# Optimization experiments

Measured on AMD Instinct MI355X. Metric: run time of the kernel, lower is better.

## Reference

```python
import jax, jax.numpy as jnp
import numpy as np

B, S, D = 2, 2048, 2048
H, HD = 16, 128  # n_heads, head_dim = dim // n_heads
NEG_INF = -1e9


def setup_inputs() -> dict:
    key = jax.random.key(0)
    ks = jax.random.split(key, 6)
    x = jax.random.normal(ks[0], (B, S, D), dtype=jnp.float32)
    # freqs_complex as (real, imag) pairs; unused downstream because the
    # source's apply_rotary_emb returns its input unchanged (x.type_as(x)).
    freqs_complex = jax.random.normal(ks[1], (S, HD // 2, 2), dtype=jnp.float32)
    # causal additive mask [1, 1, S, S]
    causal = jnp.tril(jnp.ones((S, S), dtype=bool))
    mask = jnp.where(causal, 0.0, NEG_INF).astype(jnp.float32)[None, None]
    wq = jax.random.normal(ks[2], (D, D), dtype=jnp.float32) * 0.02
    wk = jax.random.normal(ks[3], (D, D), dtype=jnp.float32) * 0.02
    wv = jax.random.normal(ks[4], (D, D), dtype=jnp.float32) * 0.02
    wo = jax.random.normal(ks[5], (D, D), dtype=jnp.float32) * 0.02
    return {"x": x, "freqs_complex": freqs_complex, "mask": mask,
            "wq": wq, "wk": wk, "wv": wv, "wo": wo}


def reference(x, freqs_complex, mask, wq, wk, wv, wo):
    b, s, d = x.shape
    # QKV projections (torch Linear: x @ W.T), reshape to [B, S, H, HD]
    q = (x @ wq.T).reshape(b, s, H, HD)
    k = (x @ wk.T).reshape(b, s, H, HD)
    v = (x @ wv.T).reshape(b, s, H, HD)
    # apply_rotary_emb in the source returns its input unchanged -> no-op.
    scale = 1.0 / jnp.sqrt(jnp.asarray(HD, dtype=x.dtype))
    scores = jnp.einsum('bshd,bthd->bhst', q, k) * scale + mask
    probs = jax.nn.softmax(scores.astype(jnp.float32), axis=-1).astype(q.dtype)
    out = jnp.einsum('bhst,bthd->bshd', probs, v).reshape(b, s, H * HD)
    return out @ wo.T
```

## Files before the change

### kernel.cpp

```cpp
#include <hip/hip_runtime.h>
#include <hip/hip_bf16.h>
#include <stdint.h>


namespace {

constexpr int kB = 2;
constexpr int kS = 2048;
constexpr int kD = 2048;
constexpr int kH = 16;
constexpr int kHD = 128;
constexpr int kM = kB * kS;

typedef __attribute__((ext_vector_type(8))) __bf16 bf16x8;
typedef __attribute__((ext_vector_type(4))) float f32x4;

__device__ __forceinline__ unsigned short f2bf(float x) {
  uint32_t u = __float_as_uint(x);
  u += 0x7fffu + ((u >> 16) & 1u);
  return (unsigned short)(u >> 16);
}

__device__ __forceinline__ void gld_lds16(const void* g, void* l) {
  __builtin_amdgcn_global_load_lds((__attribute__((address_space(1))) void*)g,
                                   (__attribute__((address_space(3))) void*)l,
                                   16, 0, 0);
}

__global__ void cvt_all(const float* __restrict__ x, const float* __restrict__ wq,
                        const float* __restrict__ wk, const float* __restrict__ wv,
                        const float* __restrict__ wo, unsigned short* __restrict__ xb,
                        unsigned short* __restrict__ wqkv) {
  constexpr int n4 = kD * kD / 4;
  const int i = blockIdx.x * blockDim.x + threadIdx.x;
  const int y = blockIdx.y;
  const float* src;
  unsigned short* dst;
  float s = 1.0f;
  if (y < 2) {
    src = x + (size_t)y * n4 * 4;
    dst = xb + (size_t)y * n4 * 4;
  } else {
    src = (y == 2) ? wq : (y == 3) ? wk : (y == 4) ? wv : wo;
    dst = wqkv + (size_t)(y - 2) * n4 * 4;
    if (y == 2) s = 0.08838834764831845f * 1.44269504088896340736f;
  }
  float4 v = ((const float4*)src)[i];
  ushort4 o;
  o.x = f2bf(v.x * s); o.y = f2bf(v.y * s); o.z = f2bf(v.z * s); o.w = f2bf(v.w * s);
  ((ushort4*)dst)[i] = o;
}

__global__ __launch_bounds__(256, 2) void gemm_qkv(
    const unsigned short* __restrict__ A, const unsigned short* __restrict__ W,
    unsigned short* __restrict__ Qb, unsigned short* __restrict__ Kb,
    unsigned short* __restrict__ Vt) {
  constexpr int K = 2048;
  __shared__ unsigned short Asm[128 * 64];
  __shared__ unsigned short Bsm[128 * 64];
  const int t = threadIdx.x;
  const int wave = t >> 6, lane = t & 63;
  const int ln = lane & 15, quad = lane >> 4;
  const int wr = wave >> 1, wc = wave & 1;
  const int m0 = blockIdx.y * 128, n0 = blockIdx.x * 128;

  const int srow = t >> 3;
  const int scol = ((t & 7) ^ (srow & 7)) << 3;
  const unsigned short* gA = A + (size_t)(m0 + srow) * K + scol;
  const unsigned short* gW = W + (size_t)(n0 + srow) * K + scol;
  const size_t g32 = (size_t)32 * K;
  unsigned short* lA = Asm + wave * 512;
  unsigned short* lB = Bsm + wave * 512;

  f32x4 acc[4][4] = {};

  for (int k0 = 0; k0 < K; k0 += 64) {
    __syncthreads();
#pragma unroll
    for (int i = 0; i < 4; ++i) {
      gld_lds16(gA + i * g32, lA + i * 2048);
      gld_lds16(gW + i * g32, lB + i * 2048);
    }
    gA += 64; gW += 64;
    __syncthreads();

#pragma unroll
    for (int kk = 0; kk < 2; ++kk) {
      bf16x8 af[4], bw[4];
#pragma unroll
      for (int mt = 0; mt < 4; ++mt) {
        const int row = wr * 64 + mt * 16 + ln;
        af[mt] = *(const bf16x8*)(Asm + row * 64 +
                                  (((kk * 4 + quad) ^ (row & 7)) << 3));
      }
#pragma unroll
      for (int nt = 0; nt < 4; ++nt) {
        const int row = wc * 64 + nt * 16 + ln;
        bw[nt] = *(const bf16x8*)(Bsm + row * 64 +
                                  (((kk * 4 + quad) ^ (row & 7)) << 3));
      }
#pragma unroll
      for (int mt = 0; mt < 4; ++mt)
#pragma unroll
        for (int nt = 0; nt < 4; ++nt)
          acc[mt][nt] = __builtin_amdgcn_mfma_f32_16x16x32_bf16(
              af[mt], bw[nt], acc[mt][nt], 0, 0, 0);
    }
  }

  const int cm = m0 + wr * 64 + quad * 4;
  const int cn = n0 + wc * 64 + ln;
  if (n0 < 4096) {
    unsigned short* dst = (n0 < 2048) ? Qb : Kb;
    const int cnl = cn & 2047;
#pragma unroll
    for (int mt = 0; mt < 4; ++mt)
#pragma unroll
      for (int r = 0; r < 4; ++r) {
        const size_t rowoff = (size_t)(cm + mt * 16 + r) * kD + cnl;
#pragma unroll
        for (int nt = 0; nt < 4; ++nt) dst[rowoff + nt * 16] = f2bf(acc[mt][nt][r]);
      }
  } else {
#pragma unroll
    for (int mt = 0; mt < 4; ++mt) {
      const int m = cm + mt * 16;
      const int bb = m >> 11, s = m & 2047;
#pragma unroll
      for (int nt = 0; nt < 4; ++nt) {
        const int d = cn + nt * 16 - 4096;
        ushort4 pk;
        pk.x = f2bf(acc[mt][nt][0]);
        pk.y = f2bf(acc[mt][nt][1]);
        pk.z = f2bf(acc[mt][nt][2]);
        pk.w = f2bf(acc[mt][nt][3]);
        *(ushort4*)&Vt[((size_t)(bb * 2048 + d)) * (size_t)kS + s] = pk;
      }
    }
  }
}

template <bool OUT_BF16>
__global__ __launch_bounds__(256, 2) void gemm_bt(
    const unsigned short* __restrict__ A, const unsigned short* __restrict__ W,
    void* __restrict__ C, int M, int N, int K) {
  __shared__ unsigned short Asm[128 * 64];
  __shared__ unsigned short Bsm[128 * 64];
  const int t = threadIdx.x;
  const int wave = t >> 6, lane = t & 63;
  const int ln = lane & 15, quad = lane >> 4;
  const int wr = wave >> 1, wc = wave & 1;
  const int m0 = blockIdx.y * 128, n0 = blockIdx.x * 128;

  const int srow = t >> 3;
  const int scol = ((t & 7) ^ (srow & 7)) << 3;
  const unsigned short* gA = A + (size_t)(m0 + srow) * K + scol;
  const unsigned short* gW = W + (size_t)(n0 + srow) * K + scol;
  const size_t g32 = (size_t)32 * K;
  unsigned short* lA = Asm + wave * 512;
  unsigned short* lB = Bsm + wave * 512;

  f32x4 acc[4][4] = {};

  for (int k0 = 0; k0 < K; k0 += 64) {
    __syncthreads();
#pragma unroll
    for (int i = 0; i < 4; ++i) {
      gld_lds16(gA + i * g32, lA + i * 2048);
      gld_lds16(gW + i * g32, lB + i * 2048);
    }
    gA += 64; gW += 64;
    __syncthreads();

#pragma unroll
    for (int kk = 0; kk < 2; ++kk) {
      bf16x8 af[4], bw[4];
#pragma unroll
      for (int mt = 0; mt < 4; ++mt) {
        const int row = wr * 64 + mt * 16 + ln;
        af[mt] = *(const bf16x8*)(Asm + row * 64 +
                                  (((kk * 4 + quad) ^ (row & 7)) << 3));
      }
#pragma unroll
      for (int nt = 0; nt < 4; ++nt) {
        const int row = wc * 64 + nt * 16 + ln;
        bw[nt] = *(const bf16x8*)(Bsm + row * 64 +
                                  (((kk * 4 + quad) ^ (row & 7)) << 3));
      }
#pragma unroll
      for (int mt = 0; mt < 4; ++mt)
#pragma unroll
        for (int nt = 0; nt < 4; ++nt)
          acc[mt][nt] = __builtin_amdgcn_mfma_f32_16x16x32_bf16(
              af[mt], bw[nt], acc[mt][nt], 0, 0, 0);
    }
  }

  const int cm = m0 + wr * 64 + quad * 4;
  const int cn = n0 + wc * 64 + ln;
#pragma unroll
  for (int mt = 0; mt < 4; ++mt)
#pragma unroll
    for (int r = 0; r < 4; ++r) {
      const size_t rowoff = (size_t)(cm + mt * 16 + r) * N + cn;
      if (OUT_BF16) {
        unsigned short* Cb = (unsigned short*)C;
#pragma unroll
        for (int nt = 0; nt < 4; ++nt) Cb[rowoff + nt * 16] = f2bf(acc[mt][nt][r]);
      } else {
        float* Cf = (float*)C;
#pragma unroll
        for (int nt = 0; nt < 4; ++nt) Cf[rowoff + nt * 16] = acc[mt][nt][r];
      }
    }
}

__global__ __launch_bounds__(256, 3) void flash_attn(
    const unsigned short* __restrict__ Q, const unsigned short* __restrict__ Kb,
    const unsigned short* __restrict__ Vt, unsigned short* __restrict__ Ob) {
  __shared__ unsigned short Ksm[64 * 128];
  __shared__ unsigned short Vsm[128 * 64];
  __shared__ unsigned short Psm[4][2048];
  const int t = threadIdx.x;
  const int wave = t >> 6, lane = t & 63;
  const int ln = lane & 15, quad = lane >> 4;
  const int bx = blockIdx.x;
  const int gq = bx >> 5;
  const int qt = (gq < 8) ? (15 - gq) : (gq - 8);
  const int bh = bx & 31, b = bh >> 4, h = bh & 15;
  const int q0 = qt * 128;

  bf16x8 qf[2][4];
#pragma unroll
  for (int st = 0; st < 2; ++st) {
    const size_t qoff =
        ((size_t)(b * kS + q0 + st * 64 + wave * 16 + ln)) * kD + h * kHD;
#pragma unroll
    for (int ks = 0; ks < 4; ++ks)
      qf[st][ks] = *(const bf16x8*)(Q + qoff + ks * 32 + quad * 8);
  }

  float lsum[2] = {0.0f, 0.0f};
  f32x4 oa[2][8] = {};

  const int krow = t >> 4;
  const unsigned short* gK =
      Kb + ((size_t)(b * kS) + krow) * kD + h * kHD + (((t & 15) ^ krow) << 3);
  const int vrow = t >> 3;
  const unsigned short* gV =
      Vt + ((size_t)(bh * 128 + vrow)) * kS + (((t & 7) ^ (vrow & 7)) << 3);

  const int nIter = 2 * qt + 2;

  for (int it = 0; it < nIter; ++it) {
    const int kv0 = it << 6;
    __syncthreads();
#pragma unroll
    for (int i = 0; i < 4; ++i)
      gld_lds16(gK + ((size_t)kv0 + i * 16) * kD, Ksm + i * 2048 + wave * 512);
#pragma unroll
    for (int i = 0; i < 4; ++i)
      gld_lds16(gV + (size_t)i * 32 * kS + kv0, Vsm + i * 2048 + wave * 512);
    __syncthreads();

    f32x4 sc[2][4] = {};
#pragma unroll
    for (int ct = 0; ct < 4; ++ct) {
      const int row = ct * 16 + ln;
#pragma unroll
      for (int ks = 0; ks < 4; ++ks) {
        bf16x8 kf =
            *(const bf16x8*)(Ksm + row * 128 + (((ks * 4 + quad) ^ ln) << 3));
#pragma unroll
        for (int st = 0; st < 2; ++st)
          sc[st][ct] = __builtin_amdgcn_mfma_f32_16x16x32_bf16(
              kf, qf[st][ks], sc[st][ct], 0, 0, 0);
      }
    }

#pragma unroll
    for (int st = 0; st < 2; ++st) {
      const int q_lo = q0 + st * 64 + wave * 16;
      const bool full = (kv0 + 63 <= q_lo);
      const int qs = q_lo + ln;
      float ls = 0.0f;
#pragma unroll
      for (int ct = 0; ct < 4; ++ct) {
        const int kvb = kv0 + ct * 16 + quad * 4;
        float p[4];
#pragma unroll
        for (int r = 0; r < 4; ++r) {
          float s = sc[st][ct][r];
          if (!full && (kvb + r > qs)) s = -1e30f;
          p[r] = exp2f(s);
          ls += p[r];
        }
        const uint32_t u0 = (uint32_t)f2bf(p[0]) | ((uint32_t)f2bf(p[1]) << 16);
        const uint32_t u1 = (uint32_t)f2bf(p[2]) | ((uint32_t)f2bf(p[3]) << 16);
        const int cs = (ct * 4 + quad) ^ (ln & 14);
        uint2 u; u.x = u0; u.y = u1;
        *(uint2*)(&Psm[wave][(st * 16 + ln) * 64 + cs * 4]) = u;
      }
      lsum[st] += ls;
    }

    bf16x8 pf[2][2];
#pragma unroll
    for (int st = 0; st < 2; ++st)
#pragma unroll
      for (int ks = 0; ks < 2; ++ks)
        pf[st][ks] = *(const bf16x8*)(
            &Psm[wave][(st * 16 + ln) * 64 +
                       (((ks * 8 + quad * 2) ^ (ln & 14)) << 2)]);
#pragma unroll
    for (int ct = 0; ct < 8; ++ct) {
      const int row = ct * 16 + ln;
#pragma unroll
      for (int ks = 0; ks < 2; ++ks) {
        bf16x8 vf =
            *(const bf16x8*)(Vsm + row * 64 + (((ks * 4 + quad) ^ (ln & 7)) << 3));
#pragma unroll
        for (int st = 0; st < 2; ++st)
          oa[st][ct] = __builtin_amdgcn_mfma_f32_16x16x32_bf16(
              pf[st][ks], vf, oa[st][ct], 0, 0, 0);
      }
    }
  }

#pragma unroll
  for (int st = 0; st < 2; ++st) {
    float l = lsum[st];
    l += __shfl_xor(l, 16, 64);
    l += __shfl_xor(l, 32, 64);
    float inv[4];
#pragma unroll
    for (int r = 0; r < 4; ++r)
      inv[r] = 1.0f / __shfl(l, (lane & 48) | (quad * 4 + r), 64);
#pragma unroll
    for (int r = 0; r < 4; ++r) {
      const size_t orow =
          ((size_t)(b * kS + q0 + st * 64 + wave * 16 + quad * 4 + r)) * kD +
          h * kHD + ln;
#pragma unroll
      for (int ct = 0; ct < 8; ++ct) Ob[orow + ct * 16] = f2bf(oa[st][ct][r] * inv[r]);
    }
  }
}

}

extern "C" void kernel_launch(void* const* d_in, const int* in_sizes, int n_in,
                              void* d_out, int out_size, void* d_ws, size_t ws_size,
                              hipStream_t stream) {
  (void)in_sizes; (void)n_in; (void)out_size; (void)ws_size;
  const float* x  = (const float*)d_in[0];
  const float* wq = (const float*)d_in[3];
  const float* wk = (const float*)d_in[4];
  const float* wv = (const float*)d_in[5];
  const float* wo = (const float*)d_in[6];
  float* out = (float*)d_out;

  unsigned short* ws   = (unsigned short*)d_ws;
  unsigned short* xb   = ws;
  unsigned short* wqkv = xb + (size_t)kM * kD;
  unsigned short* wob  = wqkv + 3 * (size_t)kD * kD;
  unsigned short* Qb   = wob + (size_t)kD * kD;
  unsigned short* Kbuf = Qb  + (size_t)kM * kD;
  unsigned short* Vt   = Kbuf + (size_t)kM * kD;
  unsigned short* Ab   = Vt + (size_t)kM * kD;

  const int n4 = kD * kD / 4;
  cvt_all<<<dim3(n4 / 256, 6), 256, 0, stream>>>(x, wq, wk, wv, wo, xb, wqkv);

  gemm_qkv<<<dim3(6144 / 128, kM / 128), 256, 0, stream>>>(xb, wqkv, Qb, Kbuf, Vt);

  flash_attn<<<dim3(512), 256, 0, stream>>>(Qb, Kbuf, Vt, Ab);

  gemm_bt<false><<<dim3(kD / 128, kM / 128), 256, 0, stream>>>(Ab, wob, out, kM, kD, kD);
}
```

Baseline: 387.9 us.

## Pair complementary causal query tiles per block to balance flash-attention work

Each attention block now handles two 64-row query tiles, j and 31-j, instead of one contiguous 128-row tile. Every block then walks a similar number of KV tiles, which evens out causal-mask load imbalance across workgroups. The lower tile's MFMA, softmax and PV work is skipped once its KV range passes the diagonal, which removes the partly masked extra tile the old scheme computed. The cost is per-iteration branching on `doSt0` and a reordered grid mapping.

```diff
diff --git a/kernel.cpp b/kernel.cpp
--- a/kernel.cpp
+++ b/kernel.cpp
@@ -225,16 +225,16 @@
   const int wave = t >> 6, lane = t & 63;
   const int ln = lane & 15, quad = lane >> 4;
   const int bx = blockIdx.x;
-  const int gq = bx >> 5;
-  const int qt = (gq < 8) ? (15 - gq) : (gq - 8);
+  const int j = bx >> 5;
   const int bh = bx & 31, b = bh >> 4, h = bh & 15;
-  const int q0 = qt * 128;
+  const int qb0 = j << 6;
+  const int qb1 = (31 - j) << 6;
 
   bf16x8 qf[2][4];
 #pragma unroll
   for (int st = 0; st < 2; ++st) {
-    const size_t qoff =
-        ((size_t)(b * kS + q0 + st * 64 + wave * 16 + ln)) * kD + h * kHD;
+    const int qb = st ? qb1 : qb0;
+    const size_t qoff = ((size_t)(b * kS + qb + wave * 16 + ln)) * kD + h * kHD;
 #pragma unroll
     for (int ks = 0; ks < 4; ++ks)
       qf[st][ks] = *(const bf16x8*)(Q + qoff + ks * 32 + quad * 8);
@@ -250,10 +250,34 @@
   const unsigned short* gV =
       Vt + ((size_t)(bh * 128 + vrow)) * kS + (((t & 7) ^ (vrow & 7)) << 3);
 
-  const int nIter = 2 * qt + 2;
-
+#define SMAX(ST, QB)                                                           \
+  {                                                                            \
+    const int q_lo = (QB) + wave * 16;                                         \
+    const bool full = (kv0 + 63 <= q_lo);                                      \
+    const int qs = q_lo + ln;                                                  \
+    float ls = 0.0f;                                                           \
+    _Pragma("unroll") for (int ct = 0; ct < 4; ++ct) {                         \
+      const int kvb = kv0 + ct * 16 + quad * 4;                                \
+      float p[4];                                                              \
+      _Pragma("unroll") for (int r = 0; r < 4; ++r) {                          \
+        float s = sc[ST][ct][r];                                               \
+        if (!full && (kvb + r > qs)) s = -1e30f;                               \
+        p[r] = exp2f(s);                                                       \
+        ls += p[r];                                                            \
+      }                                                                        \
+      const uint32_t u0 = (uint32_t)f2bf(p[0]) | ((uint32_t)f2bf(p[1]) << 16); \
+      const uint32_t u1 = (uint32_t)f2bf(p[2]) | ((uint32_t)f2bf(p[3]) << 16); \
+      const int cs = (ct * 4 + quad) ^ (ln & 14);                              \
+      uint2 u; u.x = u0; u.y = u1;                                             \
+      *(uint2*)(&Psm[wave][((ST) * 16 + ln) * 64 + cs * 4]) = u;               \
+    }                                                                          \
+    lsum[ST] += ls;                                                            \
+  }
+
+  const int nIter = 32 - j;
   for (int it = 0; it < nIter; ++it) {
     const int kv0 = it << 6;
+    const bool doSt0 = (it <= j);
     __syncthreads();
 #pragma unroll
     for (int i = 0; i < 4; ++i)
@@ -271,47 +295,24 @@
       for (int ks = 0; ks < 4; ++ks) {
         bf16x8 kf =
             *(const bf16x8*)(Ksm + row * 128 + (((ks * 4 + quad) ^ ln) << 3));
-#pragma unroll
-        for (int st = 0; st < 2; ++st)
-          sc[st][ct] = __builtin_amdgcn_mfma_f32_16x16x32_bf16(
-              kf, qf[st][ks], sc[st][ct], 0, 0, 0);
-      }
-    }
-
-#pragma unroll
-    for (int st = 0; st < 2; ++st) {
-      const int q_lo = q0 + st * 64 + wave * 16;
-      const bool full = (kv0 + 63 <= q_lo);
-      const int qs = q_lo + ln;
-      float ls = 0.0f;
-#pragma unroll
-      for (int ct = 0; ct < 4; ++ct) {
-        const int kvb = kv0 + ct * 16 + quad * 4;
-        float p[4];
-#pragma unroll
-        for (int r = 0; r < 4; ++r) {
-          float s = sc[st][ct][r];
-          if (!full && (kvb + r > qs)) s = -1e30f;
-          p[r] = exp2f(s);
-          ls += p[r];
-        }
-        const uint32_t u0 = (uint32_t)f2bf(p[0]) | ((uint32_t)f2bf(p[1]) << 16);
-        const uint32_t u1 = (uint32_t)f2bf(p[2]) | ((uint32_t)f2bf(p[3]) << 16);
-        const int cs = (ct * 4 + quad) ^ (ln & 14);
-        uint2 u; u.x = u0; u.y = u1;
-        *(uint2*)(&Psm[wave][(st * 16 + ln) * 64 + cs * 4]) = u;
-      }
-      lsum[st] += ls;
-    }
-
-    bf16x8 pf[2][2];
-#pragma unroll
-    for (int st = 0; st < 2; ++st)
-#pragma unroll
-      for (int ks = 0; ks < 2; ++ks)
-        pf[st][ks] = *(const bf16x8*)(
-            &Psm[wave][(st * 16 + ln) * 64 +
-                       (((ks * 8 + quad * 2) ^ (ln & 14)) << 2)]);
+        if (doSt0)
+          sc[0][ct] = __builtin_amdgcn_mfma_f32_16x16x32_bf16(
+              kf, qf[0][ks], sc[0][ct], 0, 0, 0);
+        sc[1][ct] = __builtin_amdgcn_mfma_f32_16x16x32_bf16(
+            kf, qf[1][ks], sc[1][ct], 0, 0, 0);
+      }
+    }
+
+    if (doSt0) SMAX(0, qb0);
+    SMAX(1, qb1);
+
+    bf16x8 pf0[2], pf1[2];
+#pragma unroll
+    for (int ks = 0; ks < 2; ++ks) {
+      const int coff = ((ks * 8 + quad * 2) ^ (ln & 14)) << 2;
+      if (doSt0) pf0[ks] = *(const bf16x8*)(&Psm[wave][(0 * 16 + ln) * 64 + coff]);
+      pf1[ks] = *(const bf16x8*)(&Psm[wave][(1 * 16 + ln) * 64 + coff]);
+    }
 #pragma unroll
     for (int ct = 0; ct < 8; ++ct) {
       const int row = ct * 16 + ln;
@@ -319,16 +320,19 @@
       for (int ks = 0; ks < 2; ++ks) {
         bf16x8 vf =
             *(const bf16x8*)(Vsm + row * 64 + (((ks * 4 + quad) ^ (ln & 7)) << 3));
-#pragma unroll
-        for (int st = 0; st < 2; ++st)
-          oa[st][ct] = __builtin_amdgcn_mfma_f32_16x16x32_bf16(
-              pf[st][ks], vf, oa[st][ct], 0, 0, 0);
-      }
-    }
-  }
+        if (doSt0)
+          oa[0][ct] = __builtin_amdgcn_mfma_f32_16x16x32_bf16(
+              pf0[ks], vf, oa[0][ct], 0, 0, 0);
+        oa[1][ct] = __builtin_amdgcn_mfma_f32_16x16x32_bf16(
+            pf1[ks], vf, oa[1][ct], 0, 0, 0);
+      }
+    }
+  }
+#undef SMAX
 
 #pragma unroll
   for (int st = 0; st < 2; ++st) {
+    const int qb = st ? qb1 : qb0;
     float l = lsum[st];
     l += __shfl_xor(l, 16, 64);
     l += __shfl_xor(l, 32, 64);
@@ -339,8 +343,7 @@
 #pragma unroll
     for (int r = 0; r < 4; ++r) {
       const size_t orow =
-          ((size_t)(b * kS + q0 + st * 64 + wave * 16 + quad * 4 + r)) * kD +
-          h * kHD + ln;
+          ((size_t)(b * kS + qb + wave * 16 + quad * 4 + r)) * kD + h * kHD + ln;
 #pragma unroll
       for (int ct = 0; ct < 8; ++ct) Ob[orow + ct * 16] = f2bf(oa[st][ct][r] * inv[r]);
     }
```

New measurement: 417.4 us. +7.6%, slower.

## Split KV range of heavy causal query tiles and merge partials in combine kernel

Applied to the files above, without the earlier changes.

Query tiles in the upper half of the causal triangle are now split into two blocks, each covering half of the KV iterations. These blocks write unnormalized fp32 partial outputs and row sums to workspace, and a new combine kernel adds the two halves, normalizes them and writes bf16. The aim is to even out per-block work across the 768-block grid and shorten the tail caused by the longest causal tiles. In exchange it adds fp32 partial-output traffic, an extra kernel launch, and reuse of workspace regions already consumed by earlier kernels.

```diff
diff --git a/kernel.cpp b/kernel.cpp
--- a/kernel.cpp
+++ b/kernel.cpp
@@ -217,7 +217,8 @@
 
 __global__ __launch_bounds__(256, 3) void flash_attn(
     const unsigned short* __restrict__ Q, const unsigned short* __restrict__ Kb,
-    const unsigned short* __restrict__ Vt, unsigned short* __restrict__ Ob) {
+    const unsigned short* __restrict__ Vt, unsigned short* __restrict__ Ob,
+    float* __restrict__ Op, float* __restrict__ Lp) {
   __shared__ unsigned short Ksm[64 * 128];
   __shared__ unsigned short Vsm[128 * 64];
   __shared__ unsigned short Psm[4][2048];
@@ -225,10 +226,23 @@
   const int wave = t >> 6, lane = t & 63;
   const int ln = lane & 15, quad = lane >> 4;
   const int bx = blockIdx.x;
-  const int gq = bx >> 5;
-  const int qt = (gq < 8) ? (15 - gq) : (gq - 8);
   const int bh = bx & 31, b = bh >> 4, h = bh & 15;
-  const int q0 = qt * 128;
+  const int cid = bx >> 5;
+
+  int qt, it0, it1, pc;
+  bool heavy;
+  if (cid < 8) {
+    qt = cid; it0 = 0; it1 = 2 * qt + 2; heavy = false; pc = 0;
+  } else {
+    const int c = cid - 8;
+    qt = 8 + (c >> 1);
+    const int half = c & 1;
+    it0 = half ? (qt + 1) : 0;
+    it1 = half ? (2 * qt + 2) : (qt + 1);
+    heavy = true;
+    pc = (bh * 8 + (qt - 8)) * 2 + half;
+  }
+  const int q0 = qt << 7;
 
   bf16x8 qf[2][4];
 #pragma unroll
@@ -250,9 +264,7 @@
   const unsigned short* gV =
       Vt + ((size_t)(bh * 128 + vrow)) * kS + (((t & 7) ^ (vrow & 7)) << 3);
 
-  const int nIter = 2 * qt + 2;
-
-  for (int it = 0; it < nIter; ++it) {
+  for (int it = it0; it < it1; ++it) {
     const int kv0 = it << 6;
     __syncthreads();
 #pragma unroll
@@ -332,18 +344,57 @@
     float l = lsum[st];
     l += __shfl_xor(l, 16, 64);
     l += __shfl_xor(l, 32, 64);
-    float inv[4];
-#pragma unroll
-    for (int r = 0; r < 4; ++r)
-      inv[r] = 1.0f / __shfl(l, (lane & 48) | (quad * 4 + r), 64);
-#pragma unroll
-    for (int r = 0; r < 4; ++r) {
-      const size_t orow =
-          ((size_t)(b * kS + q0 + st * 64 + wave * 16 + quad * 4 + r)) * kD +
-          h * kHD + ln;
-#pragma unroll
-      for (int ct = 0; ct < 8; ++ct) Ob[orow + ct * 16] = f2bf(oa[st][ct][r] * inv[r]);
-    }
+    if (!heavy) {
+      float inv[4];
+#pragma unroll
+      for (int r = 0; r < 4; ++r)
+        inv[r] = 1.0f / __shfl(l, (lane & 48) | (quad * 4 + r), 64);
+#pragma unroll
+      for (int r = 0; r < 4; ++r) {
+        const size_t orow =
+            ((size_t)(b * kS + q0 + st * 64 + wave * 16 + quad * 4 + r)) * kD +
+            h * kHD + ln;
+#pragma unroll
+        for (int ct = 0; ct < 8; ++ct)
+          Ob[orow + ct * 16] = f2bf(oa[st][ct][r] * inv[r]);
+      }
+    } else {
+      if (quad == 0) Lp[pc * 128 + st * 64 + wave * 16 + ln] = l;
+#pragma unroll
+      for (int r = 0; r < 4; ++r) {
+        const int row = st * 64 + wave * 16 + quad * 4 + r;
+        float* dst = Op + (size_t)pc * 16384 + row * 128 + ln;
+#pragma unroll
+        for (int ct = 0; ct < 8; ++ct) dst[ct * 16] = oa[st][ct][r];
+      }
+    }
+  }
+}
+
+__global__ __launch_bounds__(256) void attn_combine(
+    const float* __restrict__ Op, const float* __restrict__ Lp,
+    unsigned short* __restrict__ Ob) {
+  const int p = blockIdx.x;
+  const int bh = p >> 3, qt = 8 + (p & 7);
+  const int b = bh >> 4, h = bh & 15;
+  const int q0 = qt << 7;
+  const float* Oa = Op + (size_t)(p * 2 + 0) * 16384;
+  const float* Obp = Op + (size_t)(p * 2 + 1) * 16384;
+  const float* La = Lp + (p * 2 + 0) * 128;
+  const float* Lb = Lp + (p * 2 + 1) * 128;
+#pragma unroll
+  for (int i = 0; i < 16; ++i) {
+    const int e = (i * 256 + threadIdx.x) * 4;
+    const int row = e >> 7, d = e & 127;
+    const float4 a = *(const float4*)(Oa + e);
+    const float4 bv = *(const float4*)(Obp + e);
+    const float inv = 1.0f / (La[row] + Lb[row]);
+    ushort4 o;
+    o.x = f2bf((a.x + bv.x) * inv);
+    o.y = f2bf((a.y + bv.y) * inv);
+    o.z = f2bf((a.z + bv.z) * inv);
+    o.w = f2bf((a.w + bv.w) * inv);
+    *(ushort4*)&Ob[((size_t)(b * kS + q0 + row)) * kD + h * kHD + d] = o;
   }
 }
 
@@ -369,12 +420,17 @@
   unsigned short* Vt   = Kbuf + (size_t)kM * kD;
   unsigned short* Ab   = Vt + (size_t)kM * kD;
 
+  float* Op = (float*)d_ws;
+  float* Lp = Op + (size_t)512 * 16384;
+
   const int n4 = kD * kD / 4;
   cvt_all<<<dim3(n4 / 256, 6), 256, 0, stream>>>(x, wq, wk, wv, wo, xb, wqkv);
 
   gemm_qkv<<<dim3(6144 / 128, kM / 128), 256, 0, stream>>>(xb, wqkv, Qb, Kbuf, Vt);
 
-  flash_attn<<<dim3(512), 256, 0, stream>>>(Qb, Kbuf, Vt, Ab);
+  flash_attn<<<dim3(768), 256, 0, stream>>>(Qb, Kbuf, Vt, Ab, Op, Lp);
+
+  attn_combine<<<dim3(256), 256, 0, stream>>>(Op, Lp, Ab);
 
   gemm_bt<false><<<dim3(kD / 128, kM / 128), 256, 0, stream>>>(Ab, wob, out, kM, kD, kD);
 }
```

After: 360.9 us. 7.0% less time.
